# Optimization experiments

Measured on AMD Instinct MI355X. Metric: run time of the kernel, lower is better.

Reference implementation:

```python
import jax, jax.numpy as jnp
import numpy as np

B, H, T, OUT, MLP_H = 4096, 1024, 60, 2, 64
IN = H + 4

def setup_inputs() -> dict:
    key = jax.random.key(0)
    ks = jax.random.split(key, 12)
    s = 1.0 / np.sqrt(H)
    return {
        "z": jax.random.normal(ks[0], (B, H), jnp.float32),
        "last_vel": jax.random.normal(ks[1], (B, 2), jnp.float32),
        "last_pos": jax.random.normal(ks[2], (B, 2), jnp.float32),
        "W_ih": jax.random.uniform(ks[3], (4 * H, IN), jnp.float32, -s, s),
        "W_hh": jax.random.uniform(ks[4], (4 * H, H), jnp.float32, -s, s),
        "b_ih": jax.random.uniform(ks[5], (4 * H,), jnp.float32, -s, s),
        "b_hh": jax.random.uniform(ks[6], (4 * H,), jnp.float32, -s, s),
        "W1": jax.random.uniform(ks[7], (MLP_H, H), jnp.float32, -s, s),
        "b1": jax.random.uniform(ks[8], (MLP_H,), jnp.float32, -s, s),
        "W2": jax.random.uniform(ks[9], (OUT, MLP_H), jnp.float32, -s, s),
        "b2": jax.random.uniform(ks[10], (OUT,), jnp.float32, -s, s),
    }

def _forward(z, last_vel, last_pos, W_ih, W_hh, b_ih, b_hh, W1, b1, W2, b2):
    z_aug = jnp.concatenate([z, last_pos, last_vel], axis=-1)  # (B, H+4)
    # input is identical at every timestep -> precompute input projection once
    x_gates = z_aug @ W_ih.T + b_ih + b_hh  # (B, 4H)

    def step(carry, _):
        h, c = carry
        gates = x_gates + h @ W_hh.T  # (B, 4H)
        i, f, g, o = jnp.split(gates, 4, axis=-1)  # torch gate order i,f,g,o
        i = jax.nn.sigmoid(i)
        f = jax.nn.sigmoid(f)
        g = jnp.tanh(g)
        o = jax.nn.sigmoid(o)
        c = f * c + i * g
        h = o * jnp.tanh(c)
        return (h, c), h

    h0 = jnp.zeros((z.shape[0], W_hh.shape[1]), z.dtype)
    _, hs = jax.lax.scan(step, (h0, h0), None, length=T)  # (T, B, H)
    out = jnp.transpose(hs, (1, 0, 2))  # (B, T, H)
    delta = jax.nn.relu(out @ W1.T + b1) @ W2.T + b2  # (B, T, 2)
    return jnp.cumsum(delta, axis=1) + last_pos[:, None, :]

def reference(z, last_vel, last_pos, W_ih, W_hh, b_ih, b_hh, W1, b1, W2, b2):
    return _forward(z, last_vel, last_pos, W_ih, W_hh, b_ih, b_hh, W1, b1, W2, b2)
```

## Files before the change

kernel.cpp:

```cpp
#include <hip/hip_runtime.h>
#include <stdint.h>

#define B_    4096
#define H_    1024
#define T_    60
#define IN_   1028
#define KA_   1056
#define G4_   4096
#define MLPH_ 64
#define NB_   6

typedef __attribute__((ext_vector_type(8))) short bf16x8;
typedef __attribute__((ext_vector_type(4))) float f32x4;
typedef __attribute__((ext_vector_type(4))) unsigned short u16x4;

#define GLOBAL_AS __attribute__((address_space(1)))
#define LDS_AS    __attribute__((address_space(3)))

__device__ __forceinline__ void gload_lds16(const void* g, void* l) {
  __builtin_amdgcn_global_load_lds((GLOBAL_AS void*)const_cast<void*>(g),
                                   (LDS_AS void*)l, 16, 0, 0);
}

__device__ __forceinline__ unsigned short f2bf(float f) {
  union { float f; unsigned int u; } v; v.f = f;
  unsigned int r = v.u + 0x7FFFu + ((v.u >> 16) & 1u);
  return (unsigned short)(r >> 16);
}

__device__ __forceinline__ float bf2f(unsigned short u) {
  union { unsigned int u; float f; } v; v.u = ((unsigned int)u) << 16;
  return v.f;
}

__device__ __forceinline__ float sigmf(float x) {
  float e = __expf(-x);
  return __builtin_amdgcn_rcpf(1.0f + e);
}

__device__ __forceinline__ float tanh_fast(float x) {
  x = fminf(fmaxf(x, -15.0f), 15.0f);
  float e = __expf(2.0f * x);
  return (e - 1.0f) * __builtin_amdgcn_rcpf(e + 1.0f);
}


__global__ void k_conv_bf16(const float* __restrict__ src,
                            unsigned short* __restrict__ dst, int n) {
  int i = blockIdx.x * blockDim.x + threadIdx.x;
  int stride = gridDim.x * blockDim.x;
  for (; i < n; i += stride) dst[i] = f2bf(src[i]);
}

__global__ void k_conv_wih(const float* __restrict__ w,
                           unsigned short* __restrict__ dst) {
  int i = blockIdx.x * blockDim.x + threadIdx.x;
  int stride = gridDim.x * blockDim.x;
  const int n = G4_ * KA_;
  for (; i < n; i += stride) {
    int r = i / KA_, k = i - r * KA_;
    dst[i] = (k < IN_) ? f2bf(w[(size_t)r * IN_ + k]) : (unsigned short)0;
  }
}

__global__ void k_build_zaug(const float* __restrict__ z,
                             const float* __restrict__ lp,
                             const float* __restrict__ lv,
                             unsigned short* __restrict__ dst) {
  int i = blockIdx.x * blockDim.x + threadIdx.x;
  int stride = gridDim.x * blockDim.x;
  const int n = B_ * KA_;
  for (; i < n; i += stride) {
    int b = i / KA_, k = i - b * KA_;
    float v;
    if (k < H_)            v = z[(size_t)b * H_ + k];
    else if (k < H_ + 2)   v = lp[b * 2 + (k - H_)];
    else if (k < IN_)      v = lv[b * 2 + (k - H_ - 2)];
    else                   v = 0.0f;
    dst[i] = f2bf(v);
  }
}



__global__ __launch_bounds__(256, 4) void k_xgates(
    const unsigned short* __restrict__ zaug, const unsigned short* __restrict__ wih,
    const float* __restrict__ bih, const float* __restrict__ bhh,
    u16x4* __restrict__ xg4) {
  __shared__ unsigned short As[2][128 * 32];
  __shared__ unsigned short Bs[2][128 * 32];
  const int tid = threadIdx.x, lane = tid & 63, wave = tid >> 6;
  const int bx = blockIdx.x, by = blockIdx.y;
  const int wm = wave >> 1, wn = wave & 1;
  const int rs = lane >> 2;
  const int c16 = (((lane & 3) ^ ((lane >> 3) & 3))) * 16;
  const int rdslot = ((lane >> 4) ^ ((lane >> 1) & 3)) * 8;

  const char* asrc0 = (const char*)zaug + ((size_t)(bx * 128 + (wave * 2 + 0) * 16 + rs) * KA_) * 2 + c16;
  const char* asrc1 = (const char*)zaug + ((size_t)(bx * 128 + (wave * 2 + 1) * 16 + rs) * KA_) * 2 + c16;
  const char* bsrc0 = (const char*)wih  + ((size_t)(wave * H_ + by * 32 +  0 + rs) * KA_) * 2 + c16;
  const char* bsrc1 = (const char*)wih  + ((size_t)(wave * H_ + by * 32 + 16 + rs) * KA_) * 2 + c16;

  f32x4 acc[4][4];
#pragma unroll
  for (int g = 0; g < 4; ++g)
#pragma unroll
    for (int m = 0; m < 4; ++m) acc[g][m] = {0.f, 0.f, 0.f, 0.f};

  gload_lds16(asrc0, &As[0][(wave * 2 + 0) * 512]);
  gload_lds16(asrc1, &As[0][(wave * 2 + 1) * 512]);
  gload_lds16(bsrc0, &Bs[0][(wave * 2 + 0) * 512]);
  gload_lds16(bsrc1, &Bs[0][(wave * 2 + 1) * 512]);
  __syncthreads();

  const int nt = KA_ / 32;
  int cur = 0;
  for (int kk = 0; kk < nt; ++kk) {
    if (kk + 1 < nt) {
      const size_t kb = (size_t)(kk + 1) * 64;
      gload_lds16(asrc0 + kb, &As[cur ^ 1][(wave * 2 + 0) * 512]);
      gload_lds16(asrc1 + kb, &As[cur ^ 1][(wave * 2 + 1) * 512]);
      gload_lds16(bsrc0 + kb, &Bs[cur ^ 1][(wave * 2 + 0) * 512]);
      gload_lds16(bsrc1 + kb, &Bs[cur ^ 1][(wave * 2 + 1) * 512]);
    }
    bf16x8 a[4], b[4];
#pragma unroll
    for (int m = 0; m < 4; ++m)
      a[m] = *(const bf16x8*)&As[cur][(wm * 64 + m * 16 + (lane & 15)) * 32 + rdslot];
#pragma unroll
    for (int g = 0; g < 4; ++g)
      b[g] = *(const bf16x8*)&Bs[cur][((g * 2 + wn) * 16 + (lane & 15)) * 32 + rdslot];
#pragma unroll
    for (int g = 0; g < 4; ++g)
#pragma unroll
      for (int m = 0; m < 4; ++m)
        acc[g][m] = __builtin_amdgcn_mfma_f32_16x16x32_bf16(a[m], b[g], acc[g][m], 0, 0, 0);
    __syncthreads();
    cur ^= 1;
  }

  const int r0 = (lane >> 4) * 4, cl = lane & 15;
  const int hc = by * 32 + wn * 16 + cl;
  const float bi = bih[hc]        + bhh[hc];
  const float bf = bih[1024 + hc] + bhh[1024 + hc];
  const float bg = bih[2048 + hc] + bhh[2048 + hc];
  const float bo = bih[3072 + hc] + bhh[3072 + hc];
#pragma unroll
  for (int m = 0; m < 4; ++m)
#pragma unroll
    for (int j = 0; j < 4; ++j) {
      int row = bx * 128 + wm * 64 + m * 16 + r0 + j;
      u16x4 st = {f2bf(acc[0][m][j] + bi), f2bf(acc[1][m][j] + bf),
                  f2bf(acc[2][m][j] + bg), f2bf(acc[3][m][j] + bo)};
      xg4[(size_t)row * H_ + hc] = st;
    }
}


__global__ __launch_bounds__(256, 4) void k_step(
    const unsigned short* __restrict__ hprev, const unsigned short* __restrict__ whh,
    const u16x4* __restrict__ xg4, float* __restrict__ cbuf,
    unsigned short* __restrict__ hout) {
  __shared__ unsigned short As[2][128 * 32];
  __shared__ unsigned short Bs[2][128 * 32];
  const int tid = threadIdx.x, lane = tid & 63, wave = tid >> 6;
  const int bx = blockIdx.x, by = blockIdx.y;
  const int wm = wave >> 1, wn = wave & 1;
  const int rs = lane >> 2;
  const int c16 = (((lane & 3) ^ ((lane >> 3) & 3))) * 16;
  const int rdslot = ((lane >> 4) ^ ((lane >> 1) & 3)) * 8;

  const char* asrc0 = (const char*)hprev + ((size_t)(bx * 128 + (wave * 2 + 0) * 16 + rs) * H_) * 2 + c16;
  const char* asrc1 = (const char*)hprev + ((size_t)(bx * 128 + (wave * 2 + 1) * 16 + rs) * H_) * 2 + c16;
  const char* bsrc0 = (const char*)whh   + ((size_t)(wave * H_ + by * 32 +  0 + rs) * H_) * 2 + c16;
  const char* bsrc1 = (const char*)whh   + ((size_t)(wave * H_ + by * 32 + 16 + rs) * H_) * 2 + c16;

  f32x4 acc[4][4];
#pragma unroll
  for (int g = 0; g < 4; ++g)
#pragma unroll
    for (int m = 0; m < 4; ++m) acc[g][m] = {0.f, 0.f, 0.f, 0.f};

  gload_lds16(asrc0, &As[0][(wave * 2 + 0) * 512]);
  gload_lds16(asrc1, &As[0][(wave * 2 + 1) * 512]);
  gload_lds16(bsrc0, &Bs[0][(wave * 2 + 0) * 512]);
  gload_lds16(bsrc1, &Bs[0][(wave * 2 + 1) * 512]);
  __syncthreads();

  const int nt = H_ / 32;
  int cur = 0;
  for (int kk = 0; kk < nt; ++kk) {
    if (kk + 1 < nt) {
      const size_t kb = (size_t)(kk + 1) * 64;
      gload_lds16(asrc0 + kb, &As[cur ^ 1][(wave * 2 + 0) * 512]);
      gload_lds16(asrc1 + kb, &As[cur ^ 1][(wave * 2 + 1) * 512]);
      gload_lds16(bsrc0 + kb, &Bs[cur ^ 1][(wave * 2 + 0) * 512]);
      gload_lds16(bsrc1 + kb, &Bs[cur ^ 1][(wave * 2 + 1) * 512]);
    }
    bf16x8 a[4], b[4];
#pragma unroll
    for (int m = 0; m < 4; ++m)
      a[m] = *(const bf16x8*)&As[cur][(wm * 64 + m * 16 + (lane & 15)) * 32 + rdslot];
#pragma unroll
    for (int g = 0; g < 4; ++g)
      b[g] = *(const bf16x8*)&Bs[cur][((g * 2 + wn) * 16 + (lane & 15)) * 32 + rdslot];
#pragma unroll
    for (int g = 0; g < 4; ++g)
#pragma unroll
      for (int m = 0; m < 4; ++m)
        acc[g][m] = __builtin_amdgcn_mfma_f32_16x16x32_bf16(a[m], b[g], acc[g][m], 0, 0, 0);
    __syncthreads();
    cur ^= 1;
  }

  const int r0 = (lane >> 4) * 4, cl = lane & 15;
  const int hc = by * 32 + wn * 16 + cl;
#pragma unroll
  for (int m = 0; m < 4; ++m)
#pragma unroll
    for (int j = 0; j < 4; ++j) {
      int row = bx * 128 + wm * 64 + m * 16 + r0 + j;
      size_t ci = (size_t)row * H_ + hc;
      u16x4 xv = xg4[ci];
      float iv = sigmf(acc[0][m][j] + bf2f(xv[0]));
      float fv = sigmf(acc[1][m][j] + bf2f(xv[1]));
      float gv = tanh_fast(acc[2][m][j] + bf2f(xv[2]));
      float ov = sigmf(acc[3][m][j] + bf2f(xv[3]));
      float cv = fv * cbuf[ci] + iv * gv;
      cbuf[ci] = cv;
      hout[ci] = f2bf(ov * tanh_fast(cv));
    }
}


__global__ __launch_bounds__(256) void k_mlp(
    const unsigned short* __restrict__ hring, const unsigned short* __restrict__ w1,
    const float* __restrict__ b1, const float* __restrict__ w2,
    const float* __restrict__ b2, float* __restrict__ delta, int t0) {
  __shared__ unsigned short As[64 * 32];
  __shared__ unsigned short Bs[64 * 32];
  __shared__ float hid[64][65];
  const int tid = threadIdx.x, lane = tid & 63, wave = tid >> 6;
  const int bx = blockIdx.x;
  const unsigned short* h = hring + (size_t)blockIdx.y * B_ * H_;
  const int t = t0 + blockIdx.y;
  const int rs = lane >> 2;
  const int c16 = (((lane & 3) ^ ((lane >> 3) & 3))) * 16;
  const int rdslot = ((lane >> 4) ^ ((lane >> 1) & 3)) * 8;

  f32x4 acc[4];
#pragma unroll
  for (int n = 0; n < 4; ++n) acc[n] = {0.f, 0.f, 0.f, 0.f};

  for (int kk = 0; kk < H_ / 32; ++kk) {
    const int k0 = kk * 32;
    __syncthreads();
    {
      int row = bx * 64 + wave * 16 + rs;
      gload_lds16((const char*)h + ((size_t)row * H_ + k0) * 2 + c16,
                  (char*)As + wave * 1024);
    }
    {
      int jj = wave * 16 + rs;
      gload_lds16((const char*)w1 + ((size_t)jj * H_ + k0) * 2 + c16,
                  (char*)Bs + wave * 1024);
    }
    __syncthreads();
    bf16x8 a = *(const bf16x8*)&As[(wave * 16 + (lane & 15)) * 32 + rdslot];
#pragma unroll
    for (int n = 0; n < 4; ++n) {
      bf16x8 b = *(const bf16x8*)&Bs[(n * 16 + (lane & 15)) * 32 + rdslot];
      acc[n] = __builtin_amdgcn_mfma_f32_16x16x32_bf16(a, b, acc[n], 0, 0, 0);
    }
  }

  const int r0 = (lane >> 4) * 4, cl = lane & 15;
#pragma unroll
  for (int n = 0; n < 4; ++n)
#pragma unroll
    for (int j = 0; j < 4; ++j) {
      int row = wave * 16 + r0 + j;
      int col = n * 16 + cl;
      hid[row][col] = fmaxf(acc[n][j] + b1[col], 0.0f);
    }
  __syncthreads();

  if (tid < 128) {
    int r = tid >> 1, d = tid & 1;
    float s = b2[d];
#pragma unroll 8
    for (int k2 = 0; k2 < 64; ++k2) s += hid[r][k2] * w2[d * 64 + k2];
    delta[((size_t)(bx * 64 + r) * T_ + t) * 2 + d] = s;
  }
}


__global__ void k_cumsum(const float* __restrict__ delta,
                         const float* __restrict__ lp, float* __restrict__ out) {
  int id = blockIdx.x * blockDim.x + threadIdx.x;
  if (id >= B_ * 2) return;
  int b = id >> 1, d = id & 1;
  float cum = lp[b * 2 + d];
  size_t base = (size_t)b * T_ * 2 + d;
  for (int t = 0; t < T_; ++t) {
    cum += delta[base + t * 2];
    out[base + t * 2] = cum;
  }
}


extern "C" void kernel_launch(void* const* d_in, const int* in_sizes, int n_in,
                              void* d_out, int out_size, void* d_ws, size_t ws_size,
                              hipStream_t stream) {
  const float* z   = (const float*)d_in[0];
  const float* lv  = (const float*)d_in[1];
  const float* lp  = (const float*)d_in[2];
  const float* Wih = (const float*)d_in[3];
  const float* Whh = (const float*)d_in[4];
  const float* bih = (const float*)d_in[5];
  const float* bhh = (const float*)d_in[6];
  const float* W1  = (const float*)d_in[7];
  const float* b1  = (const float*)d_in[8];
  const float* W2  = (const float*)d_in[9];
  const float* b2  = (const float*)d_in[10];
  float* out = (float*)d_out;

  char* ws = (char*)d_ws;
  size_t off = 0;
  u16x4*          xg4    = (u16x4*)(ws + off);          off += (size_t)B_ * H_ * 8;
  unsigned short* whh_bf = (unsigned short*)(ws + off); off += (size_t)G4_ * H_ * 2;
  unsigned short* wih_bf = (unsigned short*)(ws + off); off += (size_t)G4_ * KA_ * 2;
  unsigned short* zaug   = (unsigned short*)(ws + off); off += (size_t)B_ * KA_ * 2;
  unsigned short* w1_bf  = (unsigned short*)(ws + off); off += (size_t)MLPH_ * H_ * 2;
  unsigned short* hring  = (unsigned short*)(ws + off); off += (size_t)NB_ * B_ * H_ * 2;
  float*          cbuf   = (float*)(ws + off);          off += (size_t)B_ * H_ * 4;
  float*          delta  = (float*)(ws + off);          off += (size_t)B_ * T_ * 2 * 4;

  const size_t BH = (size_t)B_ * H_;

  hipMemsetAsync(hring + (NB_ - 1) * BH, 0, BH * 2, stream);
  hipMemsetAsync(cbuf, 0, BH * 4, stream);

  k_conv_bf16 <<<2048, 256, 0, stream>>>(Whh, whh_bf, G4_ * H_);
  k_conv_wih  <<<2048, 256, 0, stream>>>(Wih, wih_bf);
  k_build_zaug<<<2048, 256, 0, stream>>>(z, lp, lv, zaug);
  k_conv_bf16 <<<256, 256, 0, stream>>>(W1, w1_bf, MLPH_ * H_);

  k_xgates<<<dim3(32, 32), 256, 0, stream>>>(zaug, wih_bf, bih, bhh, xg4);

  for (int t = 0; t < T_; ++t) {
    const unsigned short* hp = hring + (size_t)((t + NB_ - 1) % NB_) * BH;
    unsigned short*       hc = hring + (size_t)(t % NB_) * BH;
    k_step<<<dim3(32, 32), 256, 0, stream>>>(hp, whh_bf, xg4, cbuf, hc);
    if ((t % NB_) == NB_ - 1)
      k_mlp<<<dim3(64, NB_), 256, 0, stream>>>(hring, w1_bf, b1, W2, b2, delta, t - (NB_ - 1));
  }

  k_cumsum<<<32, 256, 0, stream>>>(delta, lp, out);
}
```

Measured before the change: 3.001 ms.

## Triple-buffer LSTM step GEMM with single barrier and prefetch epilogue operands

Changes the recurrent step kernel from a double-buffered LDS pipeline with two barriers per k-tile to a triple-buffered one with explicit vmcnt waits and one barrier per tile, keeping two tiles in flight. The xg4 gate preactivations and cell state are prefetched into registers during the final two k-tiles so their global latency overlaps the MFMAs. The larger LDS footprint and extra registers drop the occupancy hint from 4 to 3 blocks per CU.

```diff
diff --git a/kernel.cpp b/kernel.cpp
--- a/kernel.cpp
+++ b/kernel.cpp
@@ -157,12 +157,12 @@
 }
 
 
-__global__ __launch_bounds__(256, 4) void k_step(
+__global__ __launch_bounds__(256, 3) void k_step(
     const unsigned short* __restrict__ hprev, const unsigned short* __restrict__ whh,
     const u16x4* __restrict__ xg4, float* __restrict__ cbuf,
     unsigned short* __restrict__ hout) {
-  __shared__ unsigned short As[2][128 * 32];
-  __shared__ unsigned short Bs[2][128 * 32];
+  __shared__ unsigned short As[3][128 * 32];
+  __shared__ unsigned short Bs[3][128 * 32];
   const int tid = threadIdx.x, lane = tid & 63, wave = tid >> 6;
   const int bx = blockIdx.x, by = blockIdx.y;
   const int wm = wave >> 1, wn = wave & 1;
@@ -181,52 +181,77 @@
 #pragma unroll
     for (int m = 0; m < 4; ++m) acc[g][m] = {0.f, 0.f, 0.f, 0.f};
 
-  gload_lds16(asrc0, &As[0][(wave * 2 + 0) * 512]);
-  gload_lds16(asrc1, &As[0][(wave * 2 + 1) * 512]);
-  gload_lds16(bsrc0, &Bs[0][(wave * 2 + 0) * 512]);
-  gload_lds16(bsrc1, &Bs[0][(wave * 2 + 1) * 512]);
-  __syncthreads();
-
-  const int nt = H_ / 32;
-  int cur = 0;
-  for (int kk = 0; kk < nt; ++kk) {
-    if (kk + 1 < nt) {
-      const size_t kb = (size_t)(kk + 1) * 64;
-      gload_lds16(asrc0 + kb, &As[cur ^ 1][(wave * 2 + 0) * 512]);
-      gload_lds16(asrc1 + kb, &As[cur ^ 1][(wave * 2 + 1) * 512]);
-      gload_lds16(bsrc0 + kb, &Bs[cur ^ 1][(wave * 2 + 0) * 512]);
-      gload_lds16(bsrc1 + kb, &Bs[cur ^ 1][(wave * 2 + 1) * 512]);
-    }
+  auto stage = [&](int t, int bi) {
+    const size_t kb = (size_t)t * 64;
+    gload_lds16(asrc0 + kb, &As[bi][(wave * 2 + 0) * 512]);
+    gload_lds16(asrc1 + kb, &As[bi][(wave * 2 + 1) * 512]);
+    gload_lds16(bsrc0 + kb, &Bs[bi][(wave * 2 + 0) * 512]);
+    gload_lds16(bsrc1 + kb, &Bs[bi][(wave * 2 + 1) * 512]);
+  };
+
+  auto compute = [&](int bi) {
     bf16x8 a[4], b[4];
 #pragma unroll
     for (int m = 0; m < 4; ++m)
-      a[m] = *(const bf16x8*)&As[cur][(wm * 64 + m * 16 + (lane & 15)) * 32 + rdslot];
+      a[m] = *(const bf16x8*)&As[bi][(wm * 64 + m * 16 + (lane & 15)) * 32 + rdslot];
 #pragma unroll
     for (int g = 0; g < 4; ++g)
-      b[g] = *(const bf16x8*)&Bs[cur][((g * 2 + wn) * 16 + (lane & 15)) * 32 + rdslot];
+      b[g] = *(const bf16x8*)&Bs[bi][((g * 2 + wn) * 16 + (lane & 15)) * 32 + rdslot];
 #pragma unroll
     for (int g = 0; g < 4; ++g)
 #pragma unroll
       for (int m = 0; m < 4; ++m)
         acc[g][m] = __builtin_amdgcn_mfma_f32_16x16x32_bf16(a[m], b[g], acc[g][m], 0, 0, 0);
-    __syncthreads();
-    cur ^= 1;
+  };
+
+  stage(0, 0);
+  stage(1, 1);
+
+  int cur = 0;
+  for (int kk = 0; kk < 30; ++kk) {
+    asm volatile("s_waitcnt vmcnt(4)" ::: "memory");
+    __builtin_amdgcn_s_barrier();
+    int nb = cur + 2; if (nb >= 3) nb -= 3;
+    stage(kk + 2, nb);
+    compute(cur);
+    ++cur; if (cur == 3) cur = 0;
   }
 
   const int r0 = (lane >> 4) * 4, cl = lane & 15;
   const int hc = by * 32 + wn * 16 + cl;
+  const int browbase = bx * 128 + wm * 64 + r0;
+
+  asm volatile("s_waitcnt vmcnt(4)" ::: "memory");
+  __builtin_amdgcn_s_barrier();
+  u16x4 xpre[4][4];
 #pragma unroll
   for (int m = 0; m < 4; ++m)
 #pragma unroll
+    for (int j = 0; j < 4; ++j)
+      xpre[m][j] = xg4[(size_t)(browbase + m * 16 + j) * H_ + hc];
+  compute(0);
+
+  asm volatile("s_waitcnt vmcnt(16)" ::: "memory");
+  __builtin_amdgcn_s_barrier();
+  float cpre[4][4];
+#pragma unroll
+  for (int m = 0; m < 4; ++m)
+#pragma unroll
+    for (int j = 0; j < 4; ++j)
+      cpre[m][j] = cbuf[(size_t)(browbase + m * 16 + j) * H_ + hc];
+  compute(1);
+
+#pragma unroll
+  for (int m = 0; m < 4; ++m)
+#pragma unroll
     for (int j = 0; j < 4; ++j) {
-      int row = bx * 128 + wm * 64 + m * 16 + r0 + j;
-      size_t ci = (size_t)row * H_ + hc;
-      u16x4 xv = xg4[ci];
+      size_t ci = (size_t)(browbase + m * 16 + j) * H_ + hc;
+      u16x4 xv = xpre[m][j];
       float iv = sigmf(acc[0][m][j] + bf2f(xv[0]));
       float fv = sigmf(acc[1][m][j] + bf2f(xv[1]));
       float gv = tanh_fast(acc[2][m][j] + bf2f(xv[2]));
       float ov = sigmf(acc[3][m][j] + bf2f(xv[3]));
-      float cv = fv * cbuf[ci] + iv * gv;
+      float cv = fv * cpre[m][j] + iv * gv;
       cbuf[ci] = cv;
       hout[ci] = f2bf(ov * tanh_fast(cv));
     }
```

New measurement: 3.853 ms. +28.4%, slower.

## Enlarge LSTM step GEMM tile to 256x256 with 8-wave split-phase pipeline

Applied to the files above, without the earlier changes.

The recurrent step kernel now uses 512-thread blocks computing 256 batch rows by 64 hidden columns across all four gates, on a 16x16 grid instead of 32x32. The K loop is restructured with explicit s_barrier and vmcnt waits, split A/B staging between two MFMA halves, and setprio around the MFMA bursts so loads overlap compute. The larger tile raises operand reuse and cuts global/L2 traffic per FLOP. In exchange, the grid drops to 256 blocks, which may underfill the CUs, and accumulator register pressure doubles.

```diff
diff --git a/kernel.cpp b/kernel.cpp
--- a/kernel.cpp
+++ b/kernel.cpp
@@ -82,7 +82,6 @@
 }
 
 
-
 __global__ __launch_bounds__(256, 4) void k_xgates(
     const unsigned short* __restrict__ zaug, const unsigned short* __restrict__ wih,
     const float* __restrict__ bih, const float* __restrict__ bhh,
@@ -157,70 +156,99 @@
 }
 
 
-__global__ __launch_bounds__(256, 4) void k_step(
+#define SBAR() asm volatile("s_barrier" ::: "memory")
+
+#define MFMA_HALF(MB)                                                          \
+  _Pragma("unroll") for (int g = 0; g < 4; ++g)                                \
+  _Pragma("unroll") for (int m = 0; m < 4; ++m)                                \
+      acc[g][(MB) + m] = __builtin_amdgcn_mfma_f32_16x16x32_bf16(              \
+          a[m], b[g], acc[g][(MB) + m], 0, 0, 0);
+
+#define TILE_BODY(KT, VMS, STG)                                                \
+  {                                                                            \
+    const int c_ = (KT) & 1;                                                   \
+    if (STG) { stageA((KT) + 1, c_ ^ 1, 0); stageA((KT) + 1, c_ ^ 1, 1); }     \
+    asm volatile("s_waitcnt vmcnt(" VMS ")" ::: "memory");                     \
+    SBAR();                                                                    \
+    rdA(c_, 0); rdB(c_);                                                       \
+    __builtin_amdgcn_s_setprio(1);                                             \
+    MFMA_HALF(0)                                                               \
+    __builtin_amdgcn_s_setprio(0);                                             \
+    SBAR();                                                                    \
+    rdA(c_, 1);                                                                \
+    if (STG) { stageB((KT) + 1, c_ ^ 1, 0); stageB((KT) + 1, c_ ^ 1, 1); }     \
+    SBAR();                                                                    \
+    __builtin_amdgcn_s_setprio(1);                                             \
+    MFMA_HALF(4)                                                               \
+    __builtin_amdgcn_s_setprio(0);                                             \
+    SBAR();                                                                    \
+  }
+
+__global__ __launch_bounds__(512, 2) void k_step(
     const unsigned short* __restrict__ hprev, const unsigned short* __restrict__ whh,
     const u16x4* __restrict__ xg4, float* __restrict__ cbuf,
     unsigned short* __restrict__ hout) {
-  __shared__ unsigned short As[2][128 * 32];
-  __shared__ unsigned short Bs[2][128 * 32];
+  __shared__ unsigned short As[2][256 * 32];
+  __shared__ unsigned short Bs[2][256 * 32];
   const int tid = threadIdx.x, lane = tid & 63, wave = tid >> 6;
   const int bx = blockIdx.x, by = blockIdx.y;
-  const int wm = wave >> 1, wn = wave & 1;
-  const int rs = lane >> 2;
-  const int c16 = (((lane & 3) ^ ((lane >> 3) & 3))) * 16;
-  const int rdslot = ((lane >> 4) ^ ((lane >> 1) & 3)) * 8;
-
-  const char* asrc0 = (const char*)hprev + ((size_t)(bx * 128 + (wave * 2 + 0) * 16 + rs) * H_) * 2 + c16;
-  const char* asrc1 = (const char*)hprev + ((size_t)(bx * 128 + (wave * 2 + 1) * 16 + rs) * H_) * 2 + c16;
-  const char* bsrc0 = (const char*)whh   + ((size_t)(wave * H_ + by * 32 +  0 + rs) * H_) * 2 + c16;
-  const char* bsrc1 = (const char*)whh   + ((size_t)(wave * H_ + by * 32 + 16 + rs) * H_) * 2 + c16;
-
-  f32x4 acc[4][4];
+  const int wm = wave >> 2, wn = wave & 3;
+  const int cl = lane & 15, sl16 = lane >> 4;
+
+  const int ssrc = (lane & 3) ^ ((lane >> 2) & 3);
+  const char* aglb = (const char*)hprev +
+      ((size_t)(bx * 256 + wave * 16 + (lane >> 2)) * H_) * 2 + ssrc * 16;
+  const int bn_lo = by * 64 + (wave & 3) * 16 + (lane >> 2);
+  const char* bglb = (const char*)whh + ((size_t)bn_lo * H_) * 2 + ssrc * 16;
+  const size_t bg_off = ((size_t)(wave >> 2) * 1024) * H_ * 2;
+
+  auto stageA = [&](int kt, int c, int o) {
+    gload_lds16(aglb + (size_t)o * 128 * H_ * 2 + (size_t)kt * 64,
+                (char*)&As[c][0] + o * 8192 + wave * 1024);
+  };
+  auto stageB = [&](int kt, int c, int o) {
+    gload_lds16(bglb + bg_off + (size_t)o * 2048 * H_ * 2 + (size_t)kt * 64,
+                (char*)&Bs[c][0] + o * 8192 + wave * 1024);
+  };
+
+  const int offk = (sl16 ^ (cl & 3)) * 8;
+  const int base_a = (wm * 128 + cl) * 32;
+  const int base_b = (wn * 16 + cl) * 32;
+
+  f32x4 acc[4][8];
 #pragma unroll
   for (int g = 0; g < 4; ++g)
 #pragma unroll
-    for (int m = 0; m < 4; ++m) acc[g][m] = {0.f, 0.f, 0.f, 0.f};
-
-  gload_lds16(asrc0, &As[0][(wave * 2 + 0) * 512]);
-  gload_lds16(asrc1, &As[0][(wave * 2 + 1) * 512]);
-  gload_lds16(bsrc0, &Bs[0][(wave * 2 + 0) * 512]);
-  gload_lds16(bsrc1, &Bs[0][(wave * 2 + 1) * 512]);
-  __syncthreads();
-
-  const int nt = H_ / 32;
-  int cur = 0;
-  for (int kk = 0; kk < nt; ++kk) {
-    if (kk + 1 < nt) {
-      const size_t kb = (size_t)(kk + 1) * 64;
-      gload_lds16(asrc0 + kb, &As[cur ^ 1][(wave * 2 + 0) * 512]);
-      gload_lds16(asrc1 + kb, &As[cur ^ 1][(wave * 2 + 1) * 512]);
-      gload_lds16(bsrc0 + kb, &Bs[cur ^ 1][(wave * 2 + 0) * 512]);
-      gload_lds16(bsrc1 + kb, &Bs[cur ^ 1][(wave * 2 + 1) * 512]);
-    }
-    bf16x8 a[4], b[4];
+    for (int m = 0; m < 8; ++m) acc[g][m] = {0.f, 0.f, 0.f, 0.f};
+
+  bf16x8 a[4], b[4];
+  auto rdA = [&](int c, int mh) {
 #pragma unroll
     for (int m = 0; m < 4; ++m)
-      a[m] = *(const bf16x8*)&As[cur][(wm * 64 + m * 16 + (lane & 15)) * 32 + rdslot];
+      a[m] = *(const bf16x8*)&As[c][base_a + (mh * 4 + m) * 512 + offk];
+  };
+  auto rdB = [&](int c) {
 #pragma unroll
     for (int g = 0; g < 4; ++g)
-      b[g] = *(const bf16x8*)&Bs[cur][((g * 2 + wn) * 16 + (lane & 15)) * 32 + rdslot];
-#pragma unroll
-    for (int g = 0; g < 4; ++g)
-#pragma unroll
-      for (int m = 0; m < 4; ++m)
-        acc[g][m] = __builtin_amdgcn_mfma_f32_16x16x32_bf16(a[m], b[g], acc[g][m], 0, 0, 0);
-    __syncthreads();
-    cur ^= 1;
-  }
-
-  const int r0 = (lane >> 4) * 4, cl = lane & 15;
-  const int hc = by * 32 + wn * 16 + cl;
-#pragma unroll
-  for (int m = 0; m < 4; ++m)
+      b[g] = *(const bf16x8*)&Bs[c][base_b + g * 2048 + offk];
+  };
+
+  stageA(0, 0, 0); stageA(0, 0, 1); stageB(0, 0, 0); stageB(0, 0, 1);
+  stageA(1, 1, 0); stageA(1, 1, 1); stageB(1, 1, 0); stageB(1, 1, 1);
+
+  TILE_BODY(0, "4", false)
+  for (int kt = 1; kt <= 30; ++kt) {
+    TILE_BODY(kt, "2", true)
+  }
+  TILE_BODY(31, "0", false)
+
+  const int erow0 = bx * 256 + wm * 128 + sl16 * 4;
+  const int hc = by * 64 + wn * 16 + cl;
+#pragma unroll
+  for (int m = 0; m < 8; ++m)
 #pragma unroll
     for (int j = 0; j < 4; ++j) {
-      int row = bx * 128 + wm * 64 + m * 16 + r0 + j;
-      size_t ci = (size_t)row * H_ + hc;
+      size_t ci = (size_t)(erow0 + m * 16 + j) * H_ + hc;
       u16x4 xv = xg4[ci];
       float iv = sigmf(acc[0][m][j] + bf2f(xv[0]));
       float fv = sigmf(acc[1][m][j] + bf2f(xv[1]));
@@ -351,7 +379,7 @@
   for (int t = 0; t < T_; ++t) {
     const unsigned short* hp = hring + (size_t)((t + NB_ - 1) % NB_) * BH;
     unsigned short*       hc = hring + (size_t)(t % NB_) * BH;
-    k_step<<<dim3(32, 32), 256, 0, stream>>>(hp, whh_bf, xg4, cbuf, hc);
+    k_step<<<dim3(16, 16), 512, 0, stream>>>(hp, whh_bf, xg4, cbuf, hc);
     if ((t % NB_) == NB_ - 1)
       k_mlp<<<dim3(64, NB_), 256, 0, stream>>>(hring, w1_bf, b1, W2, b2, delta, t - (NB_ - 1));
   }
```

After: 3.045 ms. Within noise of the previous version (+1.5%).

## Enlarge LSTM step tile to 256x256 with 4-stage LDS pipeline

Applied to the files above, without the earlier changes.

Rewrites the recurrent step GEMM to use 512-thread blocks covering 256 batch rows by 64 hidden units (all four gates), with a 4-deep global-to-LDS staging ring, explicit vmcnt waits and split barriers. Each wave now computes 8x4 MFMA tiles in two halves, interleaving B-tile prefetch between them and raising wave priority around MFMA bursts. The larger tile raises arithmetic intensity and cuts redundant reloads of W_hh and h. In exchange it uses more LDS and registers per block, and the grid shrinks to 256 blocks, which risks lower occupancy and fewer blocks than there are compute units.

```diff
diff --git a/kernel.cpp b/kernel.cpp
--- a/kernel.cpp
+++ b/kernel.cpp
@@ -82,7 +82,6 @@
 }
 
 
-
 __global__ __launch_bounds__(256, 4) void k_xgates(
     const unsigned short* __restrict__ zaug, const unsigned short* __restrict__ wih,
     const float* __restrict__ bih, const float* __restrict__ bhh,
@@ -157,70 +156,95 @@
 }
 
 
-__global__ __launch_bounds__(256, 4) void k_step(
+__global__ __launch_bounds__(512, 1) void k_step(
     const unsigned short* __restrict__ hprev, const unsigned short* __restrict__ whh,
     const u16x4* __restrict__ xg4, float* __restrict__ cbuf,
     unsigned short* __restrict__ hout) {
-  __shared__ unsigned short As[2][128 * 32];
-  __shared__ unsigned short Bs[2][128 * 32];
+  __shared__ unsigned short As[4][256 * 32];
+  __shared__ unsigned short Bs[4][256 * 32];
   const int tid = threadIdx.x, lane = tid & 63, wave = tid >> 6;
   const int bx = blockIdx.x, by = blockIdx.y;
-  const int wm = wave >> 1, wn = wave & 1;
-  const int rs = lane >> 2;
-  const int c16 = (((lane & 3) ^ ((lane >> 3) & 3))) * 16;
-  const int rdslot = ((lane >> 4) ^ ((lane >> 1) & 3)) * 8;
-
-  const char* asrc0 = (const char*)hprev + ((size_t)(bx * 128 + (wave * 2 + 0) * 16 + rs) * H_) * 2 + c16;
-  const char* asrc1 = (const char*)hprev + ((size_t)(bx * 128 + (wave * 2 + 1) * 16 + rs) * H_) * 2 + c16;
-  const char* bsrc0 = (const char*)whh   + ((size_t)(wave * H_ + by * 32 +  0 + rs) * H_) * 2 + c16;
-  const char* bsrc1 = (const char*)whh   + ((size_t)(wave * H_ + by * 32 + 16 + rs) * H_) * 2 + c16;
-
-  f32x4 acc[4][4];
-#pragma unroll
-  for (int g = 0; g < 4; ++g)
-#pragma unroll
-    for (int m = 0; m < 4; ++m) acc[g][m] = {0.f, 0.f, 0.f, 0.f};
-
-  gload_lds16(asrc0, &As[0][(wave * 2 + 0) * 512]);
-  gload_lds16(asrc1, &As[0][(wave * 2 + 1) * 512]);
-  gload_lds16(bsrc0, &Bs[0][(wave * 2 + 0) * 512]);
-  gload_lds16(bsrc1, &Bs[0][(wave * 2 + 1) * 512]);
-  __syncthreads();
-
-  const int nt = H_ / 32;
-  int cur = 0;
-  for (int kk = 0; kk < nt; ++kk) {
-    if (kk + 1 < nt) {
-      const size_t kb = (size_t)(kk + 1) * 64;
-      gload_lds16(asrc0 + kb, &As[cur ^ 1][(wave * 2 + 0) * 512]);
-      gload_lds16(asrc1 + kb, &As[cur ^ 1][(wave * 2 + 1) * 512]);
-      gload_lds16(bsrc0 + kb, &Bs[cur ^ 1][(wave * 2 + 0) * 512]);
-      gload_lds16(bsrc1 + kb, &Bs[cur ^ 1][(wave * 2 + 1) * 512]);
-    }
-    bf16x8 a[4], b[4];
+  const int wm = wave >> 2, wn = wave & 3;
+  const int cl = lane & 15, sl16 = lane >> 4;
+
+  const int srow = wave * 16 + (lane >> 2);
+  const int sswz = ((lane & 3) ^ ((lane >> 2) & 3)) * 16;
+  const char* agl = (const char*)hprev + (size_t)(bx * 256 + srow) * 2048 + sswz;
+  const int hcl = (wave & 3) * 16 + (lane >> 2);
+  const int glo = wave >> 2;
+  const char* bgl = (const char*)whh + (size_t)(by * 64 + hcl) * 2048 + sswz;
+
+  auto stA = [&](int kt, int c, int o) {
+    gload_lds16(agl + (size_t)o * (128 * 2048) + (size_t)kt * 64,
+                (char*)&As[c][0] + o * 8192 + wave * 1024);
+  };
+  auto stB = [&](int kt, int c, int o) {
+    gload_lds16(bgl + ((size_t)(o * 2 + glo) << 21) + (size_t)kt * 64,
+                (char*)&Bs[c][0] + o * 8192 + wave * 1024);
+  };
+
+  const int slot8 = (sl16 ^ (cl & 3)) * 8;
+  const int aro = (wm * 128 + cl) * 32;
+  const int bro = (wn * 16 + cl) * 32;
+
+  f32x4 acc[4][8];
+#pragma unroll
+  for (int q = 0; q < 4; ++q)
+#pragma unroll
+    for (int m = 0; m < 8; ++m) acc[q][m] = {0.f, 0.f, 0.f, 0.f};
+
+  bf16x8 a[4], b[4];
+
+#pragma unroll
+  for (int p = 0; p < 3; ++p) {
+    stA(p, p, 0); stA(p, p, 1); stB(p, p, 0); stB(p, p, 1);
+  }
+
+  for (int kt = 0; kt < 32; ++kt) {
+    const int c = kt & 3, sc = (kt + 3) & 3;
+    const bool stg = (kt <= 28);
+    if (stg) { stA(kt + 3, sc, 0); stA(kt + 3, sc, 1); }
+    if (kt <= 28)      asm volatile("s_waitcnt vmcnt(10)" ::: "memory");
+    else if (kt == 29) asm volatile("s_waitcnt vmcnt(8)" ::: "memory");
+    else if (kt == 30) asm volatile("s_waitcnt vmcnt(4)" ::: "memory");
+    else               asm volatile("s_waitcnt vmcnt(0)" ::: "memory");
+    __builtin_amdgcn_s_barrier();
+#pragma unroll
+    for (int q = 0; q < 4; ++q)
+      b[q] = *(const bf16x8*)&Bs[c][bro + q * 2048 + slot8];
 #pragma unroll
     for (int m = 0; m < 4; ++m)
-      a[m] = *(const bf16x8*)&As[cur][(wm * 64 + m * 16 + (lane & 15)) * 32 + rdslot];
-#pragma unroll
-    for (int g = 0; g < 4; ++g)
-      b[g] = *(const bf16x8*)&Bs[cur][((g * 2 + wn) * 16 + (lane & 15)) * 32 + rdslot];
-#pragma unroll
-    for (int g = 0; g < 4; ++g)
+      a[m] = *(const bf16x8*)&As[c][aro + m * 512 + slot8];
+    __builtin_amdgcn_s_setprio(1);
+#pragma unroll
+    for (int q = 0; q < 4; ++q)
 #pragma unroll
       for (int m = 0; m < 4; ++m)
-        acc[g][m] = __builtin_amdgcn_mfma_f32_16x16x32_bf16(a[m], b[g], acc[g][m], 0, 0, 0);
-    __syncthreads();
-    cur ^= 1;
-  }
-
-  const int r0 = (lane >> 4) * 4, cl = lane & 15;
-  const int hc = by * 32 + wn * 16 + cl;
-#pragma unroll
-  for (int m = 0; m < 4; ++m)
+        acc[q][m] = __builtin_amdgcn_mfma_f32_16x16x32_bf16(a[m], b[q], acc[q][m], 0, 0, 0);
+    __builtin_amdgcn_s_setprio(0);
+    __builtin_amdgcn_s_barrier();
+#pragma unroll
+    for (int m = 0; m < 4; ++m)
+      a[m] = *(const bf16x8*)&As[c][aro + (4 + m) * 512 + slot8];
+    if (stg) { stB(kt + 3, sc, 0); stB(kt + 3, sc, 1); }
+    __builtin_amdgcn_s_barrier();
+    __builtin_amdgcn_s_setprio(1);
+#pragma unroll
+    for (int q = 0; q < 4; ++q)
+#pragma unroll
+      for (int m = 0; m < 4; ++m)
+        acc[q][4 + m] = __builtin_amdgcn_mfma_f32_16x16x32_bf16(a[m], b[q], acc[q][4 + m], 0, 0, 0);
+    __builtin_amdgcn_s_setprio(0);
+    __builtin_amdgcn_s_barrier();
+  }
+
+  const int erow = bx * 256 + wm * 128 + sl16 * 4;
+  const int hc = by * 64 + wn * 16 + cl;
+#pragma unroll
+  for (int m = 0; m < 8; ++m)
 #pragma unroll
     for (int j = 0; j < 4; ++j) {
-      int row = bx * 128 + wm * 64 + m * 16 + r0 + j;
-      size_t ci = (size_t)row * H_ + hc;
+      size_t ci = (size_t)(erow + m * 16 + j) * H_ + hc;
       u16x4 xv = xg4[ci];
       float iv = sigmf(acc[0][m][j] + bf2f(xv[0]));
       float fv = sigmf(acc[1][m][j] + bf2f(xv[1]));
@@ -351,7 +375,7 @@
   for (int t = 0; t < T_; ++t) {
     const unsigned short* hp = hring + (size_t)((t + NB_ - 1) % NB_) * BH;
     unsigned short*       hc = hring + (size_t)(t % NB_) * BH;
-    k_step<<<dim3(32, 32), 256, 0, stream>>>(hp, whh_bf, xg4, cbuf, hc);
+    k_step<<<dim3(16, 16), 512, 0, stream>>>(hp, whh_bf, xg4, cbuf, hc);
     if ((t % NB_) == NB_ - 1)
       k_mlp<<<dim3(64, NB_), 256, 0, stream>>>(hring, w1_bf, b1, W2, b2, delta, t - (NB_ - 1));
   }
```

After: 3.115 ms. +3.8%, slower.
